# Kernel tuning notes

Hardware: AMD Instinct MI355X
Metric: run time of the kernel (lower is better)

## Reference

```python
import jax, jax.numpy as jnp
import numpy as np

LATENT, OBS, CTRL, SEQ = 2048, 1024, 512, 4096


def setup_inputs() -> dict:
    key = jax.random.key(0)
    k1, k2, k3, k4, k5 = jax.random.split(key, 5)
    inputs = jax.random.normal(k1, (OBS, SEQ), jnp.float32)
    controls = jax.random.normal(k2, (CTRL, SEQ), jnp.float32)
    # Weight matrices (init args A, B, C of the torch module)
    Wr = jax.random.normal(k3, (LATENT, LATENT), jnp.float32) * (0.9 / np.sqrt(LATENT))
    Win = jax.random.normal(k4, (LATENT, CTRL), jnp.float32) * (1.0 / np.sqrt(CTRL))
    Wout = jax.random.normal(k5, (OBS, LATENT), jnp.float32) * (1.0 / np.sqrt(LATENT))
    return {"inputs": inputs, "controls": controls, "Wr": Wr, "Win": Win,
            "Wout": Wout, "inf_iters": 20, "inf_lr": 0.05}


def reference(inputs, controls, Wr, Win, Wout, inf_iters, inf_lr):
    """NeuralKalmanFilter.predict with nonlin='tanh', dynamic_inf=False, inf_iters>0."""
    inf_lr = jnp.float32(inf_lr)

    def step(z, xu):
        x, u = xu  # x: (OBS,), u: (CTRL,)
        # z_proj uses prev_z (the carry before inference updates)
        drive = Wr @ jnp.tanh(z) + Win @ jnp.tanh(u)  # (LATENT,)

        def inf_body(_, z):
            fz = jnp.tanh(z)
            ez = z - drive
            ex = x - Wout @ fz             # x - pred_x
            dz = ez - (1.0 - fz * fz) * (Wout.T @ ex)
            return z - inf_lr * dz

        z = jax.lax.fori_loop(0, inf_iters, inf_body, z)
        return z, (z, drive)

    z0 = jnp.zeros((LATENT,), jnp.float32)
    _, (zs, z_projs) = jax.lax.scan(step, z0, (inputs.T, controls.T))
    zs = zs.T            # (LATENT, SEQ)
    z_projs = z_projs.T  # (LATENT, SEQ)
    pred_xs = Wout @ jnp.tanh(z_projs)  # (OBS, SEQ)
    return zs, pred_xs
```

## Files before the change

### kernel.cpp

```cpp
#include <hip/hip_runtime.h>
#include <hip/hip_bf16.h>


#define SEQL 4096
#define NLAT 2048
#define NOBS 1024
#define NCTL 512

typedef unsigned short u16;
typedef unsigned int   u32;
typedef unsigned long long u64;
typedef float v2f __attribute__((ext_vector_type(2)));

__device__ __forceinline__ float bfl(u32 u)  { return __uint_as_float(u << 16); }
__device__ __forceinline__ float bfh(u32 u)  { return __uint_as_float(u & 0xffff0000u); }
__device__ __forceinline__ float bf2f(u16 s) { return __uint_as_float(((u32)s) << 16); }
__device__ __forceinline__ u16 f2bf(float f) {
  u32 x = __float_as_uint(f);
  return (u16)((x + 0x7fffu + ((x >> 16) & 1u)) >> 16);
}

#if __has_builtin(__builtin_elementwise_fma)
__device__ __forceinline__ v2f pkfma(v2f a, v2f b, v2f c) {
  return __builtin_elementwise_fma(a, b, c);
}
#else
__device__ __forceinline__ v2f pkfma(v2f a, v2f b, v2f c) {
  v2f r; r.x = fmaf(a.x, b.x, c.x); r.y = fmaf(a.y, b.y, c.y); return r;
}
#endif

__device__ __forceinline__ float fast_tanh(float x) {
#if __has_builtin(__builtin_amdgcn_exp2f) && __has_builtin(__builtin_amdgcn_rcpf)
  float e = __builtin_amdgcn_exp2f(x * 2.8853900817779268f);
  return 1.f - 2.f * __builtin_amdgcn_rcpf(e + 1.f);
#else
  return tanhf(x);
#endif
}

__global__ void k_f2b(const float* __restrict__ in, u16* __restrict__ out, int n) {
  int i = blockIdx.x * 256 + threadIdx.x;
  if (i < n) out[i] = f2bf(in[i]);
}
__global__ void k_tanh2b(const float* __restrict__ in, u16* __restrict__ out, int n) {
  int i = blockIdx.x * 256 + threadIdx.x;
  if (i < n) out[i] = f2bf(tanhf(in[i]));
}
__global__ void k_tr2b(const float* __restrict__ in, u16* __restrict__ out, int R, int C) {
  int i = blockIdx.x * 256 + threadIdx.x;
  if (i < R * C) {
    int r = i / C, c = i % C;
    out[(size_t)c * R + r] = f2bf(in[i]);
  }
}

__global__ __launch_bounds__(256) void gemm_bf16(
    const u16* __restrict__ A, const u16* __restrict__ B,
    float* __restrict__ Cf, u16* __restrict__ Cb, int M, int N, int K)
{
  __shared__ float As[32][68];
  __shared__ float Bs[32][68];
  const int tid = threadIdx.x;
  const int colBase = blockIdx.x * 64, rowBase = blockIdx.y * 64;
  const int tx = tid & 15, ty = tid >> 4;
  const int ar = tid >> 2, ak = (tid & 3) * 8;
  const int bk = tid >> 3, bc = (tid & 7) * 8;
  const u16* Ap = A + (size_t)(rowBase + ar) * K + ak;
  const u16* Bp = B + (size_t)bk * N + colBase + bc;
  float acc[4][4] = {};

  for (int k0 = 0; k0 < K; k0 += 32) {
    uint4 a = *(const uint4*)(Ap + k0);
    uint4 b = *(const uint4*)(Bp + (size_t)k0 * N);
    As[ak + 0][ar] = bfl(a.x); As[ak + 1][ar] = bfh(a.x);
    As[ak + 2][ar] = bfl(a.y); As[ak + 3][ar] = bfh(a.y);
    As[ak + 4][ar] = bfl(a.z); As[ak + 5][ar] = bfh(a.z);
    As[ak + 6][ar] = bfl(a.w); As[ak + 7][ar] = bfh(a.w);
    Bs[bk][bc + 0] = bfl(b.x); Bs[bk][bc + 1] = bfh(b.x);
    Bs[bk][bc + 2] = bfl(b.y); Bs[bk][bc + 3] = bfh(b.y);
    Bs[bk][bc + 4] = bfl(b.z); Bs[bk][bc + 5] = bfh(b.z);
    Bs[bk][bc + 6] = bfl(b.w); Bs[bk][bc + 7] = bfh(b.w);
    __syncthreads();
#pragma unroll
    for (int kk = 0; kk < 32; kk++) {
      float4 av = *(const float4*)&As[kk][ty * 4];
      float4 bv = *(const float4*)&Bs[kk][tx * 4];
      float a4[4] = {av.x, av.y, av.z, av.w};
      float b4[4] = {bv.x, bv.y, bv.z, bv.w};
#pragma unroll
      for (int i = 0; i < 4; i++)
#pragma unroll
        for (int q = 0; q < 4; q++)
          acc[i][q] = fmaf(a4[i], b4[q], acc[i][q]);
    }
    __syncthreads();
  }

  if (Cf) {
#pragma unroll
    for (int i = 0; i < 4; i++) {
      float4 v = make_float4(acc[i][0], acc[i][1], acc[i][2], acc[i][3]);
      *(float4*)&Cf[(size_t)(rowBase + ty * 4 + i) * N + colBase + tx * 4] = v;
    }
  } else {
#pragma unroll
    for (int i = 0; i < 4; i++) {
      u64 pk = (u64)f2bf(acc[i][0]) | ((u64)f2bf(acc[i][1]) << 16) |
               ((u64)f2bf(acc[i][2]) << 32) | ((u64)f2bf(acc[i][3]) << 48);
      *(u64*)&Cb[(size_t)(rowBase + ty * 4 + i) * N + colBase + tx * 4] = pk;
    }
  }
}

__global__ void __launch_bounds__(256, 1)
scan_kernel(const u16* __restrict__ G,
            const u16* __restrict__ Wr,
            const u16* __restrict__ Bmat,
            const u16* __restrict__ Cin,
            float* __restrict__ zs,
            u16* __restrict__ td,
            u64* __restrict__ fzbuf,
            const int* __restrict__ itp, const float* __restrict__ lrp)
{
  __shared__ __align__(16) float fzLDS[NLAT];
  __shared__ float corrLDS[8], wrLDS[8];
  __shared__ int sAbort;

  const int tid = threadIdx.x, bid = blockIdx.x;
  const int lane = tid & 63, wave = tid >> 6;
  const int row_local = wave * 2 + (lane >> 5);
  const int chunk = lane & 31;
  const int row = bid * 8 + row_local;
  const int row8 = bid * 8 + lane;

  const int niters = *itp;
  const float lr = *lrp;

#if __has_builtin(__builtin_amdgcn_s_setprio)
  if (wave == 0) __builtin_amdgcn_s_setprio(1);
#endif

  uint2 wGp[16], wWp[16];
  {
    const u16* gRow = G  + (size_t)row * NLAT + chunk * 4;
    const u16* wRow = Wr + (size_t)row * NLAT + chunk * 4;
#pragma unroll
    for (int i = 0; i < 16; i++) {
      wGp[i] = *(const uint2*)(gRow + 128 * i);
      wWp[i] = *(const uint2*)(wRow + 128 * i);
    }
  }
  for (int i = tid; i < NLAT; i += 256) fzLDS[i] = 0.f;
  if (tid == 0) sAbort = 0;

  const int w0 = tid, w1 = tid + 256, w2 = tid + 512;
  float* o0; float* o1; float* o2; int s0_, s1_, s2_;
  {
    int b0 = w0 / 3; s0_ = w0 - b0 * 3; o0 = fzLDS + b0 * 8 + s0_ * 3;
    int b1 = w1 / 3; s1_ = w1 - b1 * 3; o1 = fzLDS + b1 * 8 + s1_ * 3;
    int b2 = w2 / 3; s2_ = w2 - b2 * 3; o2 = fzLDS + b2 * 8 + s2_ * 3;
  }

  float z = 0.f, fz = 0.f, drive = 0.f, bv = 0.f;
  float bvN = 0.f, cvN = 0.f;
  if (wave == 0 && lane < 8) {
    bvN = bf2f(Bmat[(size_t)row8 * SEQL]);
    cvN = bf2f(Cin [(size_t)row8 * SEQL]);
  }
  __syncthreads();

  u32 p = 0;
  for (int t = 0; t < SEQL; t++) {
    for (int j = 0; j < niters; j++) {
      p++;
      v2f aG = {0.f, 0.f}, aW = {0.f, 0.f};
      const float4* f4 = (const float4*)(fzLDS + chunk * 4);
      if (j == 0) {
#pragma unroll
        for (int i = 0; i < 16; i++) {
          float4 v = f4[32 * i];
          uint2 g = wGp[i], w = wWp[i];
          v2f vlo = {v.x, v.y}, vhi = {v.z, v.w};
          aG = pkfma((v2f){bfl(g.x), bfh(g.x)}, vlo, aG);
          aG = pkfma((v2f){bfl(g.y), bfh(g.y)}, vhi, aG);
          aW = pkfma((v2f){bfl(w.x), bfh(w.x)}, vlo, aW);
          aW = pkfma((v2f){bfl(w.y), bfh(w.y)}, vhi, aW);
        }
      } else {
#pragma unroll
        for (int i = 0; i < 16; i++) {
          float4 v = f4[32 * i];
          uint2 g = wGp[i];
          aG = pkfma((v2f){bfl(g.x), bfh(g.x)}, (v2f){v.x, v.y}, aG);
          aG = pkfma((v2f){bfl(g.y), bfh(g.y)}, (v2f){v.z, v.w}, aG);
        }
      }
      float accG = aG.x + aG.y, accW = aW.x + aW.y;
#pragma unroll
      for (int m = 16; m; m >>= 1) accG += __shfl_xor(accG, m, 64);
      if (j == 0) {
#pragma unroll
        for (int m = 16; m; m >>= 1) accW += __shfl_xor(accW, m, 64);
      }
      if (chunk == 0) {
        corrLDS[row_local] = accG;
        if (j == 0) wrLDS[row_local] = accW;
      }
      __syncthreads();

      if (wave == 0) {
        u32 myfz = 0;
        if (lane < 8) {
          if (j == 0) { bv = bvN; drive = wrLDS[lane] + cvN; }
          float corr = bv - corrLDS[lane];
          float dz = (z - drive) - (1.f - fz * fz) * corr;
          z -= lr * dz;
          fz = fast_tanh(z);
          myfz = f2bf(fz);
        }
        int slot = lane % 3;
        u32 a = __shfl((int)myfz, 3 * slot, 64);
        u32 b = __shfl((int)myfz, 3 * slot + 1, 64);
        u32 c = __shfl((int)myfz, 3 * slot + 2, 64);
        if (lane < 24) {
          int rep = lane / 3;
          u64 word = (u64)(u16)p | ((u64)a << 16) | ((u64)b << 32) | ((u64)c << 48);
          __hip_atomic_store(
              &fzbuf[((size_t)(p & 1) * 8 + rep) * 768 + bid * 3 + slot], word,
              __ATOMIC_RELAXED, __HIP_MEMORY_SCOPE_AGENT);
        }
        if (lane < 8) {
          if (j == 0) {
            td[(size_t)row8 * SEQL + t] = f2bf(fast_tanh(drive));
            int tn = t + 1 < SEQL ? t + 1 : t;
            bvN = bf2f(Bmat[(size_t)row8 * SEQL + tn]);
            cvN = bf2f(Cin [(size_t)row8 * SEQL + tn]);
          }
          if (j == niters - 1) zs[(size_t)row8 * SEQL + t] = z;
        }
      }

      const u64* base = fzbuf + ((size_t)(p & 1) * 8 + (bid & 7)) * 768;
      u16 want = (u16)p;
      u64 g0 = __hip_atomic_load(base + w0, __ATOMIC_RELAXED, __HIP_MEMORY_SCOPE_AGENT);
      u64 g1 = __hip_atomic_load(base + w1, __ATOMIC_RELAXED, __HIP_MEMORY_SCOPE_AGENT);
      u64 g2 = __hip_atomic_load(base + w2, __ATOMIC_RELAXED, __HIP_MEMORY_SCOPE_AGENT);
      int guard = 0;
      while ((u16)g0 != want || (u16)g1 != want || (u16)g2 != want) {
        if (++guard > 2000000) { sAbort = 1; break; }
#if __has_builtin(__builtin_amdgcn_s_sleep)
        __builtin_amdgcn_s_sleep(1);
#endif
        if ((u16)g0 != want)
          g0 = __hip_atomic_load(base + w0, __ATOMIC_RELAXED, __HIP_MEMORY_SCOPE_AGENT);
        if ((u16)g1 != want)
          g1 = __hip_atomic_load(base + w1, __ATOMIC_RELAXED, __HIP_MEMORY_SCOPE_AGENT);
        if ((u16)g2 != want)
          g2 = __hip_atomic_load(base + w2, __ATOMIC_RELAXED, __HIP_MEMORY_SCOPE_AGENT);
      }

      o0[0] = bf2f((u16)(g0 >> 16)); o0[1] = bf2f((u16)(g0 >> 32));
      if (s0_ != 2) o0[2] = bf2f((u16)(g0 >> 48));
      o1[0] = bf2f((u16)(g1 >> 16)); o1[1] = bf2f((u16)(g1 >> 32));
      if (s1_ != 2) o1[2] = bf2f((u16)(g1 >> 48));
      o2[0] = bf2f((u16)(g2 >> 16)); o2[1] = bf2f((u16)(g2 >> 32));
      if (s2_ != 2) o2[2] = bf2f((u16)(g2 >> 48));
      __syncthreads();
      if (sAbort) return;
    }
  }
}

extern "C" void kernel_launch(void* const* d_in, const int* in_sizes, int n_in,
                              void* d_out, int out_size, void* d_ws, size_t ws_size,
                              hipStream_t stream)
{
  const float* inputs   = (const float*)d_in[0];
  const float* controls = (const float*)d_in[1];
  const float* Wr       = (const float*)d_in[2];
  const float* Win      = (const float*)d_in[3];
  const float* Wout     = (const float*)d_in[4];
  const int*   itp      = (const int*)d_in[5];
  const float* lrp      = (const float*)d_in[6];
  float* out = (float*)d_out;
  char* ws = (char*)d_ws;

  size_t off = 0;
  u16*   WrB   = (u16*)(ws + off);   off += (size_t)NLAT * NLAT * 2;
  u16*   Gb    = (u16*)(ws + off);   off += (size_t)NLAT * NLAT * 2;
  u16*   WoutB = (u16*)(ws + off);   off += (size_t)NOBS * NLAT * 2;
  u16*   WinB  = (u16*)(ws + off);   off += (size_t)NLAT * NCTL * 2;
  u16*   XB    = (u16*)(ws + off);   off += (size_t)NOBS * SEQL * 2;
  u16*   UB    = (u16*)(ws + off);   off += (size_t)NCTL * SEQL * 2;
  u16*   WoutT = (u16*)(ws + off);   off += (size_t)NLAT * NOBS * 2;
  u16*   CinB  = (u16*)(ws + off);   off += (size_t)NLAT * SEQL * 2;
  u16*   TD    = (u16*)(ws + off);   off += (size_t)NLAT * SEQL * 2;
  u64*   fzbuf = (u64*)(ws + off);   off += (size_t)2 * 8 * 768 * 8;

  float* zs   = out;
  float* pred = out + (size_t)NLAT * SEQL;
  u16* BmatB  = (u16*)pred;

  k_f2b   <<<(NLAT * NLAT + 255) / 256, 256, 0, stream>>>(Wr,    WrB,   NLAT * NLAT);
  k_f2b   <<<(NOBS * NLAT + 255) / 256, 256, 0, stream>>>(Wout,  WoutB, NOBS * NLAT);
  k_f2b   <<<(NLAT * NCTL + 255) / 256, 256, 0, stream>>>(Win,   WinB,  NLAT * NCTL);
  k_f2b   <<<(NOBS * SEQL + 255) / 256, 256, 0, stream>>>(inputs, XB,   NOBS * SEQL);
  k_tanh2b<<<(NCTL * SEQL + 255) / 256, 256, 0, stream>>>(controls, UB, NCTL * SEQL);
  k_tr2b  <<<(NOBS * NLAT + 255) / 256, 256, 0, stream>>>(Wout, WoutT, NOBS, NLAT);

  gemm_bf16<<<dim3(NLAT / 64, NLAT / 64), 256, 0, stream>>>(WoutT, WoutB, nullptr, Gb,
                                                            NLAT, NLAT, NOBS);
  gemm_bf16<<<dim3(SEQL / 64, NLAT / 64), 256, 0, stream>>>(WoutT, XB, nullptr, BmatB,
                                                            NLAT, SEQL, NOBS);
  gemm_bf16<<<dim3(SEQL / 64, NLAT / 64), 256, 0, stream>>>(WinB, UB, nullptr, CinB,
                                                            NLAT, SEQL, NCTL);

  const u16* Gc = Gb; const u16* Wrc = WrB; const u16* Bc = BmatB; const u16* Cc = CinB;
  float* zsp = zs; u16* tdp = TD; u64* fzp = fzbuf;
  const int* it = itp; const float* lr = lrp;
  void* args[9] = { &Gc, &Wrc, &Bc, &Cc, &zsp, &tdp, &fzp, &it, &lr };
  hipLaunchCooperativeKernel((void*)scan_kernel, dim3(NLAT / 8), dim3(256), args, 0, stream);

  gemm_bf16<<<dim3(SEQL / 64, NOBS / 64), 256, 0, stream>>>(WoutB, TD, pred, nullptr,
                                                            NOBS, SEQL, NLAT);
}
```

Before: 211.6 ms.

## Remove intra-block barrier by updating latents per wave and double-buffering fz

Each wave half now performs the z update for its own row right after a DPP-accelerated reduction, which removes the mid-iteration __syncthreads and the single-wave serialization of updates. The fz vector is double-buffered in LDS, and each block writes its own values locally so it can skip polling its own slots. The fzbuf layout changes to two values per word with four words per block, and the buffer is zeroed before launch. The poll loop keeps three loads in flight at a time and uses a lower abort guard. The cost is more global stores per iteration and more redundant polling loads.

```diff
diff --git a/kernel.cpp b/kernel.cpp
--- a/kernel.cpp
+++ b/kernel.cpp
@@ -39,6 +39,28 @@
 #endif
 }
 
+template <int CTRL>
+__device__ __forceinline__ float dpp_add(float x) {
+#if __has_builtin(__builtin_amdgcn_update_dpp)
+  int y = __builtin_amdgcn_update_dpp(0, __float_as_int(x), CTRL, 0xF, 0xF, true);
+  return x + __int_as_float(y);
+#else
+  return x + __shfl_xor(x, (CTRL == 0xB1) ? 1 : 2, 64);
+#endif
+}
+__device__ __forceinline__ float red32(float x) {
+  x = dpp_add<0xB1>(x);
+  x = dpp_add<0x4E>(x);
+  x += __shfl_xor(x, 4, 64);
+  x += __shfl_xor(x, 8, 64);
+  x += __shfl_xor(x, 16, 64);
+  return x;
+}
+
+__device__ __forceinline__ u64 LDW(const u64* p) {
+  return __hip_atomic_load(p, __ATOMIC_RELAXED, __HIP_MEMORY_SCOPE_AGENT);
+}
+
 __global__ void k_f2b(const float* __restrict__ in, u16* __restrict__ out, int n) {
   int i = blockIdx.x * 256 + threadIdx.x;
   if (i < n) out[i] = f2bf(in[i]);
@@ -53,6 +75,10 @@
     int r = i / C, c = i % C;
     out[(size_t)c * R + r] = f2bf(in[i]);
   }
+}
+__global__ void k_zero(u64* __restrict__ p, int n) {
+  int i = blockIdx.x * 256 + threadIdx.x;
+  if (i < n) p[i] = 0ull;
 }
 
 __global__ __launch_bounds__(256) void gemm_bf16(
@@ -123,149 +149,136 @@
             u64* __restrict__ fzbuf,
             const int* __restrict__ itp, const float* __restrict__ lrp)
 {
-  __shared__ __align__(16) float fzLDS[NLAT];
-  __shared__ float corrLDS[8], wrLDS[8];
+  __shared__ __align__(16) float fzL[2][NLAT];
   __shared__ int sAbort;
 
   const int tid = threadIdx.x, bid = blockIdx.x;
-  const int lane = tid & 63, wave = tid >> 6;
-  const int row_local = wave * 2 + (lane >> 5);
+  const int lane = tid & 63, wv = tid >> 6;
+  const int h = lane >> 5;
   const int chunk = lane & 31;
-  const int row = bid * 8 + row_local;
-  const int row8 = bid * 8 + lane;
+  const int myrow = (bid << 3) + (wv << 1) + h;
 
   const int niters = *itp;
   const float lr = *lrp;
 
-#if __has_builtin(__builtin_amdgcn_s_setprio)
-  if (wave == 0) __builtin_amdgcn_s_setprio(1);
-#endif
-
   uint2 wGp[16], wWp[16];
   {
-    const u16* gRow = G  + (size_t)row * NLAT + chunk * 4;
-    const u16* wRow = Wr + (size_t)row * NLAT + chunk * 4;
+    const u16* gRow = G  + (size_t)myrow * NLAT + chunk * 4;
+    const u16* wRow = Wr + (size_t)myrow * NLAT + chunk * 4;
 #pragma unroll
     for (int i = 0; i < 16; i++) {
       wGp[i] = *(const uint2*)(gRow + 128 * i);
       wWp[i] = *(const uint2*)(wRow + 128 * i);
     }
   }
-  for (int i = tid; i < NLAT; i += 256) fzLDS[i] = 0.f;
+  for (int i = tid; i < 2 * NLAT; i += 256) (&fzL[0][0])[i] = 0.f;
   if (tid == 0) sAbort = 0;
 
-  const int w0 = tid, w1 = tid + 256, w2 = tid + 512;
-  float* o0; float* o1; float* o2; int s0_, s1_, s2_;
-  {
-    int b0 = w0 / 3; s0_ = w0 - b0 * 3; o0 = fzLDS + b0 * 8 + s0_ * 3;
-    int b1 = w1 / 3; s1_ = w1 - b1 * 3; o1 = fzLDS + b1 * 8 + s1_ * 3;
-    int b2 = w2 / 3; s2_ = w2 - b2 * 3; o2 = fzLDS + b2 * 8 + s2_ * 3;
-  }
+  const int w0 = tid, w1 = tid + 256, w2 = tid + 512, w3 = tid + 768;
+  const bool sk0 = (w0 >> 2) == bid, sk1 = (w1 >> 2) == bid,
+             sk2 = (w2 >> 2) == bid, sk3 = (w3 >> 2) == bid;
 
   float z = 0.f, fz = 0.f, drive = 0.f, bv = 0.f;
-  float bvN = 0.f, cvN = 0.f;
-  if (wave == 0 && lane < 8) {
-    bvN = bf2f(Bmat[(size_t)row8 * SEQL]);
-    cvN = bf2f(Cin [(size_t)row8 * SEQL]);
-  }
+  float bvN = bf2f(Bmat[(size_t)myrow * SEQL]);
+  float cvN = bf2f(Cin [(size_t)myrow * SEQL]);
   __syncthreads();
 
   u32 p = 0;
   for (int t = 0; t < SEQL; t++) {
     for (int j = 0; j < niters; j++) {
       p++;
-      v2f aG = {0.f, 0.f}, aW = {0.f, 0.f};
-      const float4* f4 = (const float4*)(fzLDS + chunk * 4);
+      const int wb = p & 1, rb = wb ^ 1;
+      v2f aG0 = {0.f,0.f}, aG1 = {0.f,0.f}, aG2 = {0.f,0.f}, aG3 = {0.f,0.f};
+      const float4* f4 = (const float4*)(&fzL[rb][chunk * 4]);
+      float accW = 0.f;
       if (j == 0) {
-#pragma unroll
-        for (int i = 0; i < 16; i++) {
-          float4 v = f4[32 * i];
-          uint2 g = wGp[i], w = wWp[i];
-          v2f vlo = {v.x, v.y}, vhi = {v.z, v.w};
-          aG = pkfma((v2f){bfl(g.x), bfh(g.x)}, vlo, aG);
-          aG = pkfma((v2f){bfl(g.y), bfh(g.y)}, vhi, aG);
-          aW = pkfma((v2f){bfl(w.x), bfh(w.x)}, vlo, aW);
-          aW = pkfma((v2f){bfl(w.y), bfh(w.y)}, vhi, aW);
+        v2f aW0 = {0.f,0.f}, aW1 = {0.f,0.f};
+#pragma unroll
+        for (int i = 0; i < 16; i += 2) {
+          float4 va = f4[32 * i], vb = f4[32 * (i + 1)];
+          uint2 ga = wGp[i], gb = wGp[i + 1];
+          uint2 wa = wWp[i], wbm = wWp[i + 1];
+          v2f va0 = {va.x, va.y}, va1 = {va.z, va.w};
+          v2f vb0 = {vb.x, vb.y}, vb1 = {vb.z, vb.w};
+          aG0 = pkfma((v2f){bfl(ga.x), bfh(ga.x)}, va0, aG0);
+          aG1 = pkfma((v2f){bfl(ga.y), bfh(ga.y)}, va1, aG1);
+          aG2 = pkfma((v2f){bfl(gb.x), bfh(gb.x)}, vb0, aG2);
+          aG3 = pkfma((v2f){bfl(gb.y), bfh(gb.y)}, vb1, aG3);
+          aW0 = pkfma((v2f){bfl(wa.x), bfh(wa.x)}, va0, aW0);
+          aW0 = pkfma((v2f){bfl(wa.y), bfh(wa.y)}, va1, aW0);
+          aW1 = pkfma((v2f){bfl(wbm.x), bfh(wbm.x)}, vb0, aW1);
+          aW1 = pkfma((v2f){bfl(wbm.y), bfh(wbm.y)}, vb1, aW1);
         }
+        v2f aW = aW0 + aW1;
+        accW = red32(aW.x + aW.y);
       } else {
 #pragma unroll
-        for (int i = 0; i < 16; i++) {
-          float4 v = f4[32 * i];
-          uint2 g = wGp[i];
-          aG = pkfma((v2f){bfl(g.x), bfh(g.x)}, (v2f){v.x, v.y}, aG);
-          aG = pkfma((v2f){bfl(g.y), bfh(g.y)}, (v2f){v.z, v.w}, aG);
+        for (int i = 0; i < 16; i += 2) {
+          float4 va = f4[32 * i], vb = f4[32 * (i + 1)];
+          uint2 ga = wGp[i], gb = wGp[i + 1];
+          aG0 = pkfma((v2f){bfl(ga.x), bfh(ga.x)}, (v2f){va.x, va.y}, aG0);
+          aG1 = pkfma((v2f){bfl(ga.y), bfh(ga.y)}, (v2f){va.z, va.w}, aG1);
+          aG2 = pkfma((v2f){bfl(gb.x), bfh(gb.x)}, (v2f){vb.x, vb.y}, aG2);
+          aG3 = pkfma((v2f){bfl(gb.y), bfh(gb.y)}, (v2f){vb.z, vb.w}, aG3);
         }
       }
-      float accG = aG.x + aG.y, accW = aW.x + aW.y;
-#pragma unroll
-      for (int m = 16; m; m >>= 1) accG += __shfl_xor(accG, m, 64);
+      v2f aG = (aG0 + aG1) + (aG2 + aG3);
+      float accG = red32(aG.x + aG.y);
+
+      if (j == 0) { bv = bvN; drive = accW + cvN; }
+      float corr = bv - accG;
+      float dz = (z - drive) - (1.f - fz * fz) * corr;
+      z -= lr * dz;
+      fz = fast_tanh(z);
+      u32 mybf = f2bf(fz);
+      u32 otbf = (u32)__shfl_xor((int)mybf, 32, 64) & 0xffffu;
+      u32 loB = h ? otbf : mybf;
+      u32 hiB = h ? mybf : otbf;
+      u64 word = (u64)(u16)p | ((u64)loB << 16) | ((u64)hiB << 32);
+      if (lane < 8) {
+        u64* dst = fzbuf + ((size_t)wb * 8 + lane) * 1024 + (bid << 2) + wv;
+        __hip_atomic_store(dst, word, __ATOMIC_RELAXED, __HIP_MEMORY_SCOPE_AGENT);
+      }
+      if (lane == 0)
+        ((float2*)fzL[wb])[(bid << 2) + wv] =
+            make_float2(bf2f((u16)loB), bf2f((u16)hiB));
+
       if (j == 0) {
-#pragma unroll
-        for (int m = 16; m; m >>= 1) accW += __shfl_xor(accW, m, 64);
+        if (chunk == 0) td[(size_t)myrow * SEQL + t] = f2bf(fast_tanh(drive));
+        int tn = t + 1 < SEQL ? t + 1 : t;
+        bvN = bf2f(Bmat[(size_t)myrow * SEQL + tn]);
+        cvN = bf2f(Cin [(size_t)myrow * SEQL + tn]);
       }
-      if (chunk == 0) {
-        corrLDS[row_local] = accG;
-        if (j == 0) wrLDS[row_local] = accW;
-      }
-      __syncthreads();
-
-      if (wave == 0) {
-        u32 myfz = 0;
-        if (lane < 8) {
-          if (j == 0) { bv = bvN; drive = wrLDS[lane] + cvN; }
-          float corr = bv - corrLDS[lane];
-          float dz = (z - drive) - (1.f - fz * fz) * corr;
-          z -= lr * dz;
-          fz = fast_tanh(z);
-          myfz = f2bf(fz);
-        }
-        int slot = lane % 3;
-        u32 a = __shfl((int)myfz, 3 * slot, 64);
-        u32 b = __shfl((int)myfz, 3 * slot + 1, 64);
-        u32 c = __shfl((int)myfz, 3 * slot + 2, 64);
-        if (lane < 24) {
-          int rep = lane / 3;
-          u64 word = (u64)(u16)p | ((u64)a << 16) | ((u64)b << 32) | ((u64)c << 48);
-          __hip_atomic_store(
-              &fzbuf[((size_t)(p & 1) * 8 + rep) * 768 + bid * 3 + slot], word,
-              __ATOMIC_RELAXED, __HIP_MEMORY_SCOPE_AGENT);
-        }
-        if (lane < 8) {
-          if (j == 0) {
-            td[(size_t)row8 * SEQL + t] = f2bf(fast_tanh(drive));
-            int tn = t + 1 < SEQL ? t + 1 : t;
-            bvN = bf2f(Bmat[(size_t)row8 * SEQL + tn]);
-            cvN = bf2f(Cin [(size_t)row8 * SEQL + tn]);
-          }
-          if (j == niters - 1) zs[(size_t)row8 * SEQL + t] = z;
-        }
-      }
-
-      const u64* base = fzbuf + ((size_t)(p & 1) * 8 + (bid & 7)) * 768;
+      if (j == niters - 1 && chunk == 0) zs[(size_t)myrow * SEQL + t] = z;
+
+      const u64* base = fzbuf + ((size_t)wb * 8 + (bid & 7)) * 1024;
       u16 want = (u16)p;
-      u64 g0 = __hip_atomic_load(base + w0, __ATOMIC_RELAXED, __HIP_MEMORY_SCOPE_AGENT);
-      u64 g1 = __hip_atomic_load(base + w1, __ATOMIC_RELAXED, __HIP_MEMORY_SCOPE_AGENT);
-      u64 g2 = __hip_atomic_load(base + w2, __ATOMIC_RELAXED, __HIP_MEMORY_SCOPE_AGENT);
+      u64 g0 = LDW(base + w0), g1 = LDW(base + w1),
+          g2 = LDW(base + w2), g3 = LDW(base + w3);
+      u64 h0 = LDW(base + w0), h1 = LDW(base + w1),
+          h2 = LDW(base + w2), h3 = LDW(base + w3);
+      u64 k0 = LDW(base + w0), k1 = LDW(base + w1),
+          k2 = LDW(base + w2), k3 = LDW(base + w3);
       int guard = 0;
-      while ((u16)g0 != want || (u16)g1 != want || (u16)g2 != want) {
-        if (++guard > 2000000) { sAbort = 1; break; }
+      for (;;) {
+        bool ok = (sk0 || (u16)g0 == want) && (sk1 || (u16)g1 == want) &&
+                  (sk2 || (u16)g2 == want) && (sk3 || (u16)g3 == want);
+        if (ok) break;
+        if (++guard > 400000) { sAbort = 1; break; }
 #if __has_builtin(__builtin_amdgcn_s_sleep)
         __builtin_amdgcn_s_sleep(1);
 #endif
-        if ((u16)g0 != want)
-          g0 = __hip_atomic_load(base + w0, __ATOMIC_RELAXED, __HIP_MEMORY_SCOPE_AGENT);
-        if ((u16)g1 != want)
-          g1 = __hip_atomic_load(base + w1, __ATOMIC_RELAXED, __HIP_MEMORY_SCOPE_AGENT);
-        if ((u16)g2 != want)
-          g2 = __hip_atomic_load(base + w2, __ATOMIC_RELAXED, __HIP_MEMORY_SCOPE_AGENT);
+        g0 = h0; g1 = h1; g2 = h2; g3 = h3;
+        h0 = k0; h1 = k1; h2 = k2; h3 = k3;
+        k0 = LDW(base + w0); k1 = LDW(base + w1);
+        k2 = LDW(base + w2); k3 = LDW(base + w3);
       }
 
-      o0[0] = bf2f((u16)(g0 >> 16)); o0[1] = bf2f((u16)(g0 >> 32));
-      if (s0_ != 2) o0[2] = bf2f((u16)(g0 >> 48));
-      o1[0] = bf2f((u16)(g1 >> 16)); o1[1] = bf2f((u16)(g1 >> 32));
-      if (s1_ != 2) o1[2] = bf2f((u16)(g1 >> 48));
-      o2[0] = bf2f((u16)(g2 >> 16)); o2[1] = bf2f((u16)(g2 >> 32));
-      if (s2_ != 2) o2[2] = bf2f((u16)(g2 >> 48));
+      float2* dstL = (float2*)fzL[wb];
+      if (!sk0) dstL[w0] = make_float2(bf2f((u16)(g0 >> 16)), bf2f((u16)(g0 >> 32)));
+      if (!sk1) dstL[w1] = make_float2(bf2f((u16)(g1 >> 16)), bf2f((u16)(g1 >> 32)));
+      if (!sk2) dstL[w2] = make_float2(bf2f((u16)(g2 >> 16)), bf2f((u16)(g2 >> 32)));
+      if (!sk3) dstL[w3] = make_float2(bf2f((u16)(g3 >> 16)), bf2f((u16)(g3 >> 32)));
       __syncthreads();
       if (sAbort) return;
     }
@@ -296,7 +309,7 @@
   u16*   WoutT = (u16*)(ws + off);   off += (size_t)NLAT * NOBS * 2;
   u16*   CinB  = (u16*)(ws + off);   off += (size_t)NLAT * SEQL * 2;
   u16*   TD    = (u16*)(ws + off);   off += (size_t)NLAT * SEQL * 2;
-  u64*   fzbuf = (u64*)(ws + off);   off += (size_t)2 * 8 * 768 * 8;
+  u64*   fzbuf = (u64*)(ws + off);   off += (size_t)2 * 8 * 1024 * 8;
 
   float* zs   = out;
   float* pred = out + (size_t)NLAT * SEQL;
@@ -308,6 +321,7 @@
   k_f2b   <<<(NOBS * SEQL + 255) / 256, 256, 0, stream>>>(inputs, XB,   NOBS * SEQL);
   k_tanh2b<<<(NCTL * SEQL + 255) / 256, 256, 0, stream>>>(controls, UB, NCTL * SEQL);
   k_tr2b  <<<(NOBS * NLAT + 255) / 256, 256, 0, stream>>>(Wout, WoutT, NOBS, NLAT);
+  k_zero  <<<(2 * 8 * 1024 + 255) / 256, 256, 0, stream>>>(fzbuf, 2 * 8 * 1024);
 
   gemm_bf16<<<dim3(NLAT / 64, NLAT / 64), 256, 0, stream>>>(WoutT, WoutB, nullptr, Gb,
                                                             NLAT, NLAT, NOBS);
```

Result: slower. 341.0 ms (+61.1%).
